# Optimization experiments

Measured on AMD Instinct MI355X. Metric: run time of the kernel, lower is better.

The kernel has to match this reference:

```python
import jax, jax.numpy as jnp
import numpy as np

NUM_HEADS = 8
NUM_Q = 64
RANK = 64
DIM = 768
LN_EPS = 1e-5


def setup_inputs() -> dict:
    key = jax.random.key(0)
    ks = jax.random.split(key, 8)
    b, n = 4, 1024
    x = jax.random.normal(ks[0], (b, NUM_Q, DIM), dtype=jnp.float32)
    context = jax.random.normal(ks[1], (b, n, DIM), dtype=jnp.float32)
    s = 0.02
    Wq = jax.random.normal(ks[2], (DIM, DIM), dtype=jnp.float32) * s
    Wk = jax.random.normal(ks[3], (DIM, DIM), dtype=jnp.float32) * s
    Wv1 = jax.random.normal(ks[4], (DIM, NUM_Q * RANK), dtype=jnp.float32) * s
    ln_g = jnp.ones((NUM_Q * RANK,), dtype=jnp.float32)
    ln_b = jnp.zeros((NUM_Q * RANK,), dtype=jnp.float32)
    Wc = jax.random.normal(ks[5], (NUM_Q, RANK, DIM), dtype=jnp.float32) * s
    Wout = jax.random.normal(ks[6], (DIM, DIM), dtype=jnp.float32) * s
    return {"x": x, "context": context, "Wq": Wq, "Wk": Wk, "Wv1": Wv1,
            "ln_g": ln_g, "ln_b": ln_b, "Wc": Wc, "Wout": Wout}


def reference(x, context, Wq, Wk, Wv1, ln_g, ln_b, Wc, Wout):
    b, nq, d = x.shape
    n = context.shape[1]
    h, dh = NUM_HEADS, d // NUM_HEADS

    q = x @ Wq                      # [b, nq, d]
    k = context @ Wk                # [b, n, d]

    # q-aware V: Linear -> LayerNorm(all_q_mid) -> grouped 1x1 conv (per-query rank->d)
    h1 = context @ Wv1              # [b, n, NUM_Q*RANK]
    mu = jnp.mean(h1, axis=-1, keepdims=True)
    var = jnp.var(h1, axis=-1, keepdims=True)
    h1 = (h1 - mu) * jax.lax.rsqrt(var + LN_EPS) * ln_g + ln_b
    vmid = h1.reshape(b, n, NUM_Q, RANK)
    v = jnp.einsum('bnqr,qrd->bqnd', vmid, Wc)   # [b, NUM_Q, n, d]
    # split heads: 'b q n (h dh) -> b h q n dh'
    v = v.reshape(b, NUM_Q, n, h, dh).transpose(0, 3, 1, 2, 4)

    qh = q.reshape(b, nq, h, dh).transpose(0, 2, 1, 3)   # [b,h,nq,dh]
    kh = k.reshape(b, n, h, dh).transpose(0, 2, 1, 3)    # [b,h,n,dh]
    scale = dh ** (-0.25)
    sim = jnp.einsum('bhid,bhjd->bhij', qh * scale, kh * scale)
    attn = jax.nn.softmax(sim, axis=-1)                  # [b,h,nq,n]
    out = jnp.einsum('bhij,bhijd->bhid', attn, v)        # per-query V
    out = out.transpose(0, 2, 1, 3).reshape(b, nq, d)
    return out @ Wout
```

## Files before the change

### kernel.cpp

```cpp
#include <hip/hip_runtime.h>
#include <math.h>

typedef unsigned short ushort_t;
typedef __bf16 bf16x8 __attribute__((ext_vector_type(8)));
typedef float f32x4 __attribute__((ext_vector_type(4)));

__device__ __forceinline__ ushort_t f2b_rne(float f) {
    union { float f; unsigned int u; } c;
    c.f = f;
    unsigned int u = c.u;
    u += 0x7FFFu + ((u >> 16) & 1u);
    return (ushort_t)(u >> 16);
}
__device__ __forceinline__ float b2f(ushort_t v) {
    union { unsigned int u; float f; } c;
    c.u = ((unsigned int)v) << 16;
    return c.f;
}

__device__ __forceinline__ void gl_lds16(const ushort_t* g, ushort_t* l) {
    __builtin_amdgcn_global_load_lds(
        (const __attribute__((address_space(1))) void*)g,
        (__attribute__((address_space(3))) void*)l, 16, 0, 0);
}

__global__ __launch_bounds__(256) void prep(
    const float* __restrict__ x, const float* __restrict__ context,
    const float* __restrict__ Wq, const float* __restrict__ Wk,
    const float* __restrict__ Wv1, const float* __restrict__ Wout,
    ushort_t* __restrict__ x_b, ushort_t* __restrict__ ctx_b,
    ushort_t* __restrict__ Wq_t, ushort_t* __restrict__ Wk_t,
    ushort_t* __restrict__ Wv1_t, ushort_t* __restrict__ Wout_b,
    float* __restrict__ colzero,
    int b, int n) {
    const int t = threadIdx.x;
    const int bid = blockIdx.x;
    const int nb_x = (b * 64 * 768 / 4) / 256;
    const int nb_c = (b * n * 768 / 4) / 256;

    if (bid < nb_x + nb_c) {
        const float* in = (bid < nb_x) ? x : context;
        ushort_t* outp = (bid < nb_x) ? x_b : ctx_b;
        const int i = ((bid < nb_x) ? bid : (bid - nb_x)) * 256 + t;
        float4 v = ((const float4*)in)[i];
        ushort_t o[4] = {f2b_rne(v.x), f2b_rne(v.y), f2b_rne(v.z), f2b_rne(v.w)};
        *(uint2*)&outp[(size_t)i * 4] = *(uint2*)o;
        return;
    }

    int u = bid - nb_x - nb_c;
    if (u >= 4800) {
        const int idx = (u - 4800) * 256 + t;
        ((float4*)colzero)[idx] = make_float4(0.f, 0.f, 0.f, 0.f);
        return;
    }
    if (u >= 4224) {
        const int i = (u - 4224) * 256 + t;
        float4 v = ((const float4*)Wout)[i];
        ushort_t o[4] = {f2b_rne(v.x), f2b_rne(v.y), f2b_rne(v.z), f2b_rne(v.w)};
        *(uint2*)&Wout_b[(size_t)i * 4] = *(uint2*)o;
        return;
    }

    const float* in;
    ushort_t* outp;
    int R = 768, C = 768;
    if (u < 576)        { in = Wq;  outp = Wq_t; }
    else if (u < 1152)  { u -= 576;  in = Wk;  outp = Wk_t; }
    else                { u -= 1152; in = Wv1; outp = Wv1_t; C = 4096; }
    const int ct = C / 32;
    const int c0 = (u % ct) * 32, r0 = (u / ct) * 32;
    const int tx = t & 31, ty = t >> 5;

    __shared__ float tt[32][33];
#pragma unroll
    for (int i = 0; i < 4; i++)
        tt[ty + 8 * i][tx] = in[(size_t)(r0 + ty + 8 * i) * C + c0 + tx];
    __syncthreads();
#pragma unroll
    for (int i = 0; i < 4; i++)
        outp[(size_t)(c0 + ty + 8 * i) * R + r0 + tx] = f2b_rne(tt[tx][ty + 8 * i]);
}

__global__ __launch_bounds__(256) void gemm3(
    const ushort_t* __restrict__ x_b, const ushort_t* __restrict__ ctx_b,
    const ushort_t* __restrict__ Wq_t, const ushort_t* __restrict__ Wk_t,
    const ushort_t* __restrict__ Wv1_t,
    ushort_t* __restrict__ qb, ushort_t* __restrict__ kb,
    ushort_t* __restrict__ h1t, int b, int n) {
    const int bid = blockIdx.x;
    const int tq = (b * 64 / 128) * 6;
    const int tk = (b * n / 128) * 6;
    const int Mn = b * n;

    const ushort_t *A, *Bt;
    ushort_t* C;
    int N, row0, col0;
    if (bid < tq) {
        A = x_b; Bt = Wq_t; C = qb; N = 768;
        row0 = (bid / 6) * 128; col0 = (bid % 6) * 128;
    } else if (bid < tq + tk) {
        const int u = bid - tq;
        A = ctx_b; Bt = Wk_t; C = kb; N = 768;
        row0 = (u / 6) * 128; col0 = (u % 6) * 128;
    } else {
        const int u = bid - tq - tk;
        A = Wv1_t; Bt = ctx_b; C = h1t; N = Mn;
        row0 = (u % 32) * 128; col0 = (u / 32) * 128;
    }
    const int K = 768;

    __shared__ ushort_t As[2 * 128 * 32];
    __shared__ ushort_t Bs[2 * 128 * 32];

    const int t = threadIdx.x;
    const int lane = t & 63;
    const int wave = t >> 6;
    const int quad = lane >> 4;
    const int l15 = lane & 15;
    const int wm = (wave >> 1) * 64;
    const int wn = (wave & 1) * 64;

    const ushort_t* gA0 = A + (size_t)(row0 + (t >> 2)) * K + (t & 3) * 8;
    const ushort_t* gA1 = gA0 + (size_t)64 * K;
    const ushort_t* gB0 = Bt + (size_t)(col0 + (t >> 2)) * K + (t & 3) * 8;
    const ushort_t* gB1 = gB0 + (size_t)64 * K;

    ushort_t* lA0 = &As[wave * 512];
    ushort_t* lA1 = &As[2048 + wave * 512];
    ushort_t* lA2 = &As[4096 + wave * 512];
    ushort_t* lA3 = &As[6144 + wave * 512];
    ushort_t* lB0 = &Bs[wave * 512];
    ushort_t* lB1 = &Bs[2048 + wave * 512];
    ushort_t* lB2 = &Bs[4096 + wave * 512];
    ushort_t* lB3 = &Bs[6144 + wave * 512];

    f32x4 acc[4][4] = {};

    for (int k0 = 0; k0 < K; k0 += 64) {
        __syncthreads();
        gl_lds16(gA0 + k0, lA0);
        gl_lds16(gA1 + k0, lA1);
        gl_lds16(gA0 + k0 + 32, lA2);
        gl_lds16(gA1 + k0 + 32, lA3);
        gl_lds16(gB0 + k0, lB0);
        gl_lds16(gB1 + k0, lB1);
        gl_lds16(gB0 + k0 + 32, lB2);
        gl_lds16(gB1 + k0 + 32, lB3);
        __syncthreads();

#pragma unroll
        for (int ks = 0; ks < 2; ks++) {
            bf16x8 af[4], bfr[4];
#pragma unroll
            for (int i = 0; i < 4; i++)
                af[i] = *(const bf16x8*)&As[ks * 4096 + (wm + i * 16 + l15) * 32 + quad * 8];
#pragma unroll
            for (int j = 0; j < 4; j++)
                bfr[j] = *(const bf16x8*)&Bs[ks * 4096 + (wn + j * 16 + l15) * 32 + quad * 8];
#pragma unroll
            for (int i = 0; i < 4; i++)
#pragma unroll
                for (int j = 0; j < 4; j++)
                    acc[i][j] = __builtin_amdgcn_mfma_f32_16x16x32_bf16(
                        af[i], bfr[j], acc[i][j], 0, 0, 0);
        }
    }

#pragma unroll
    for (int i = 0; i < 4; i++)
#pragma unroll
        for (int j = 0; j < 4; j++)
#pragma unroll
            for (int r = 0; r < 4; r++) {
                const int row = row0 + wm + i * 16 + quad * 4 + r;
                const int col = col0 + wn + j * 16 + l15;
                C[(size_t)row * N + col] = f2b_rne(acc[i][j][r]);
            }
}

__global__ __launch_bounds__(256) void scores_stats(
    const ushort_t* __restrict__ qb, const ushort_t* __restrict__ kb,
    const ushort_t* __restrict__ h1t, float* __restrict__ S,
    float* __restrict__ colsum, float* __restrict__ colsumsq,
    int b, int n, int Mn) {
    __shared__ ushort_t sb[192 * 104];
    const int t = threadIdx.x;
    const int nsc = b * 8 * (n / 128);

    if (blockIdx.x >= nsc) {
        const int u = blockIdx.x - nsc;
        const int rc = u >> 4;
        const int cc = u & 15;
        const int cg = t & 31;
        const int rg = t >> 5;
        const ushort_t* p =
            h1t + (size_t)(rc * 256 + rg * 32) * Mn + cc * 256 + cg * 8;
        float s[8] = {}, s2[8] = {};
#pragma unroll 4
        for (int r = 0; r < 32; r++) {
            const bf16x8 v = *(const bf16x8*)&p[(size_t)r * Mn];
#pragma unroll
            for (int j = 0; j < 8; j++) {
                const float f = (float)v[j];
                s[j] += f;
                s2[j] += f * f;
            }
        }
        float* red = (float*)sb;
#pragma unroll
        for (int j = 0; j < 8; j++) {
            red[rg * 256 + cg * 8 + j] = s[j];
            red[2048 + rg * 256 + cg * 8 + j] = s2[j];
        }
        __syncthreads();
        float ts = 0.f, ts2 = 0.f;
#pragma unroll
        for (int g = 0; g < 8; g++) {
            ts += red[g * 256 + t];
            ts2 += red[2048 + g * 256 + t];
        }
        atomicAdd(&colsum[cc * 256 + t], ts);
        atomicAdd(&colsumsq[cc * 256 + t], ts2);
        return;
    }

    const int nt = n / 128;
    const int n0 = (blockIdx.x % nt) * 128;
    const int bh = blockIdx.x / nt;
    const int bb = bh >> 3, h = bh & 7;
    const int lane = t & 63, wave = t >> 6;
    const int quad = lane >> 4, l15 = lane & 15;
    const int wm = (wave >> 1) * 32;
    const int wn = (wave & 1) * 64;

    ushort_t* Qs = sb;
    ushort_t* Ks = sb + 64 * 104;

    for (int g = t; g < 768; g += 256) {
        const int r = g / 12, s = g - r * 12;
        *(bf16x8*)&Qs[r * 104 + s * 8] =
            *(const bf16x8*)&qb[(size_t)(bb * 64 + r) * 768 + h * 96 + s * 8];
    }
    for (int g = t; g < 1536; g += 256) {
        const int r = g / 12, s = g - r * 12;
        *(bf16x8*)&Ks[r * 104 + s * 8] =
            *(const bf16x8*)&kb[(size_t)(bb * n + n0 + r) * 768 + h * 96 + s * 8];
    }
    __syncthreads();

    f32x4 acc[2][4] = {};
#pragma unroll
    for (int ks = 0; ks < 3; ks++) {
        bf16x8 af[2], bfr[4];
#pragma unroll
        for (int i = 0; i < 2; i++)
            af[i] = *(const bf16x8*)&Qs[(wm + i * 16 + l15) * 104 + ks * 32 + quad * 8];
#pragma unroll
        for (int j = 0; j < 4; j++)
            bfr[j] = *(const bf16x8*)&Ks[(wn + j * 16 + l15) * 104 + ks * 32 + quad * 8];
#pragma unroll
        for (int i = 0; i < 2; i++)
#pragma unroll
            for (int j = 0; j < 4; j++)
                acc[i][j] = __builtin_amdgcn_mfma_f32_16x16x32_bf16(
                    af[i], bfr[j], acc[i][j], 0, 0, 0);
    }

    const float sc = 0.10206207261596575f;
    float* Sp = S + (size_t)bh * 64 * n;
#pragma unroll
    for (int i = 0; i < 2; i++)
#pragma unroll
        for (int j = 0; j < 4; j++)
#pragma unroll
            for (int r = 0; r < 4; r++) {
                const int row = wm + i * 16 + quad * 4 + r;
                const int col = n0 + wn + j * 16 + l15;
                Sp[(size_t)row * n + col] = acc[i][j][r] * sc;
            }
}

__global__ __launch_bounds__(1024) void attn_fused(
    const float* __restrict__ S, const float* __restrict__ colsum,
    const float* __restrict__ colsumsq, const ushort_t* __restrict__ h1t,
    const float* __restrict__ ln_g, const float* __restrict__ ln_b,
    const float* __restrict__ Wc, const ushort_t* __restrict__ Wout_b,
    float* __restrict__ out, int n, int Mn) {
    const int bq = blockIdx.x;
    const int bb = bq >> 6, qi = bq & 63;
    const int tid = threadIdx.x;
    const int lane = tid & 63, wv = tid >> 6;
    const int quad = lane >> 4, l15 = lane & 15;

    __shared__ ushort_t sW[9 * 1032];
    __shared__ ushort_t sH[64 * 264];
    __shared__ float sl[8], swmu[8];
    __shared__ float pm[16], pl[16], pwm[16];
    __shared__ float sA[512];
    __shared__ float sO[768];

    float* sMu = (float*)sH;
    float* sRs = (float*)sH + 1024;

    for (int i = tid; i < n; i += 1024) {
        const float cs = colsum[bb * n + i];
        const float cq = colsumsq[bb * n + i];
        const float m = cs * (1.0f / 4096.0f);
        sMu[i] = m;
        sRs[i] = rsqrtf(cq * (1.0f / 4096.0f) - m * m + 1e-5f);
    }
    for (int i = tid; i < 1032; i += 1024) sW[8 * 1032 + i] = 0;
    __syncthreads();

    const int h = wv >> 1;
    const int half = wv & 1;
    const int nh = n >> 1;
    const int i0 = half * nh;
    const float* Sp = S + ((size_t)(bb * 8 + h) * 64 + qi) * n;
    {
        float m = -1e30f;
        for (int i = i0 + lane; i < i0 + nh; i += 64) m = fmaxf(m, Sp[i]);
#pragma unroll
        for (int off = 32; off > 0; off >>= 1) m = fmaxf(m, __shfl_down(m, off));
        if (lane == 0) pm[wv] = m;
    }
    __syncthreads();
    const float mh = fmaxf(pm[2 * h], pm[2 * h + 1]);
    {
        float l = 0.f, wm = 0.f;
        for (int i = i0 + lane; i < i0 + nh; i += 64) {
            const float e = expf(Sp[i] - mh);
            const float w = e * sRs[i];
            const ushort_t wb = f2b_rne(w);
            sW[h * 1032 + i] = wb;
            l += e;
            wm += b2f(wb) * sMu[i];
        }
#pragma unroll
        for (int off = 32; off > 0; off >>= 1) {
            l += __shfl_down(l, off);
            wm += __shfl_down(wm, off);
        }
        if (lane == 0) { pl[wv] = l; pwm[wv] = wm; }
    }
    __syncthreads();
    if (tid < 8) {
        sl[tid] = pl[2 * tid] + pl[2 * tid + 1];
        swmu[tid] = pwm[2 * tid] + pwm[2 * tid + 1];
    }

    const int mrow = (l15 < 8 ? l15 : 8) * 1032;
    f32x4 acc = {};
    const int nch = n >> 8;
    for (int ch = 0; ch < nch; ch++) {
        __syncthreads();
        for (int g = tid; g < 2048; g += 1024) {
            const int row = g >> 5, seg = g & 31;
            *(bf16x8*)&sH[row * 264 + seg * 8] =
                *(const bf16x8*)&h1t[(size_t)(qi * 64 + row) * Mn + bb * n +
                                     ch * 256 + seg * 8];
        }
        __syncthreads();
        if (wv < 4) {
#pragma unroll
            for (int ks = 0; ks < 8; ks++) {
                const bf16x8 af = *(const bf16x8*)&sW[mrow + ch * 256 + ks * 32 + quad * 8];
                const bf16x8 bf = *(const bf16x8*)&sH[(wv * 16 + l15) * 264 + ks * 32 + quad * 8];
                acc = __builtin_amdgcn_mfma_f32_16x16x32_bf16(af, bf, acc, 0, 0, 0);
            }
        }
    }
    __syncthreads();

    if (wv < 4) {
#pragma unroll
        for (int r = 0; r < 4; r++) {
            const int hh = quad * 4 + r;
            if (hh < 8) {
                const int rr = wv * 16 + l15;
                const int c = qi * 64 + rr;
                sA[hh * 64 + rr] =
                    ln_g[c] * ((acc[r] - swmu[hh]) / sl[hh]) + ln_b[c];
            }
        }
    }
    __syncthreads();

    for (int d = tid; d < 768; d += 1024) {
        const int hh = d / 96;
        const float* wp = Wc + (size_t)qi * 49152 + d;
        float a = 0.f;
#pragma unroll
        for (int r = 0; r < 64; r++) a += sA[hh * 64 + r] * wp[(size_t)r * 768];
        sO[d] = b2f(f2b_rne(a));
    }
    __syncthreads();

    float* rbuf = (float*)sH;
    if (tid < 768) {
        const int r0 = tid / 96;
        const int c0 = (tid % 96) * 8;
        const ushort_t* wp = Wout_b + (size_t)(r0 * 96) * 768 + c0;
        float acc8[8] = {};
#pragma unroll 4
        for (int s = 0; s < 96; s++) {
            const float sv = sO[r0 * 96 + s];
            const bf16x8 w8 = *(const bf16x8*)&wp[(size_t)s * 768];
#pragma unroll
            for (int j = 0; j < 8; j++) acc8[j] += sv * (float)w8[j];
        }
#pragma unroll
        for (int j = 0; j < 8; j++) rbuf[r0 * 768 + c0 + j] = acc8[j];
    }
    __syncthreads();
    if (tid < 768) {
        float s = 0.f;
#pragma unroll
        for (int g = 0; g < 8; g++) s += rbuf[g * 768 + tid];
        out[(size_t)bq * 768 + tid] = s;
    }
}

extern "C" void kernel_launch(void* const* d_in, const int* in_sizes, int n_in,
                              void* d_out, int out_size, void* d_ws, size_t ws_size,
                              hipStream_t stream) {
    const float* x       = (const float*)d_in[0];
    const float* context = (const float*)d_in[1];
    const float* Wq      = (const float*)d_in[2];
    const float* Wk      = (const float*)d_in[3];
    const float* Wv1     = (const float*)d_in[4];
    const float* ln_g    = (const float*)d_in[5];
    const float* ln_b    = (const float*)d_in[6];
    const float* Wc      = (const float*)d_in[7];
    const float* Wout    = (const float*)d_in[8];
    float* out = (float*)d_out;

    const int b = in_sizes[0] / (64 * 768);
    const int n = in_sizes[1] / (b * 768);
    const int M  = b * 64;
    const int Mn = b * n;

    float* ws = (float*)d_ws;
    size_t off = 0;
    float* S       = ws + off;  off += (size_t)b * 8 * 64 * n;
    float* colsum  = ws + off;  off += (size_t)Mn;
    float* colsumsq= ws + off;  off += (size_t)Mn;

    ushort_t* us = (ushort_t*)(ws + off);
    size_t uo = 0;
    ushort_t* x_b    = us + uo;  uo += (size_t)M * 768;
    ushort_t* ctx_b  = us + uo;  uo += (size_t)Mn * 768;
    ushort_t* qb     = us + uo;  uo += (size_t)M * 768;
    ushort_t* kb     = us + uo;  uo += (size_t)Mn * 768;
    ushort_t* h1t    = us + uo;  uo += (size_t)Mn * 4096;
    ushort_t* Wq_t   = us + uo;  uo += (size_t)768 * 768;
    ushort_t* Wk_t   = us + uo;  uo += (size_t)768 * 768;
    ushort_t* Wv1_t  = us + uo;  uo += (size_t)4096 * 768;
    ushort_t* Wout_b = us + uo;  uo += (size_t)768 * 768;

    const int nb_x = (M * 768 / 4) / 256;
    const int nb_c = (Mn * 768 / 4) / 256;
    prep<<<nb_x + nb_c + 4800 + 8, 256, 0, stream>>>(
        x, context, Wq, Wk, Wv1, Wout, x_b, ctx_b, Wq_t, Wk_t, Wv1_t, Wout_b,
        colsum, b, n);

    const int tq = (M / 128) * 6, tk = (Mn / 128) * 6;
    const int th = (4096 / 128) * (Mn / 128);
    gemm3<<<tq + tk + th, 256, 0, stream>>>(x_b, ctx_b, Wq_t, Wk_t, Wv1_t,
                                            qb, kb, h1t, b, n);

    scores_stats<<<b * 8 * (n / 128) + 256, 256, 0, stream>>>(
        qb, kb, h1t, S, colsum, colsumsq, b, n, Mn);

    attn_fused<<<M, 1024, 0, stream>>>(S, colsum, colsumsq, h1t, ln_g, ln_b,
                                       Wc, Wout_b, out, n, Mn);
}
```

Baseline: 169.7 us.

## Rewrite projection GEMMs with 4-slot LDS ring pipeline and 256x256 tiles

Replaces the double-barrier 128x128 GEMM with a templated tile routine that streams K in 32-wide stages through a four-slot LDS ring, prefetching three stages ahead with explicit vmcnt waits. The big h1 projection uses 256x256 tiles with 512 threads, and the LDS layout is XOR-swizzled to reduce bank conflicts. The aim is to hide global-to-LDS latency and raise MFMA utilisation. In exchange it needs 128KB of dynamic LDS and relies on hand-set wait counts that must match the number of outstanding loads.

```diff
diff --git a/kernel.cpp b/kernel.cpp
--- a/kernel.cpp
+++ b/kernel.cpp
@@ -82,101 +82,141 @@
         outp[(size_t)(c0 + ty + 8 * i) * R + r0 + tx] = f2b_rne(tt[tx][ty + 8 * i]);
 }
 
-__global__ __launch_bounds__(256) void gemm3(
+template <int BM, int BN>
+__device__ __forceinline__ void gemm_tile(
+    const ushort_t* __restrict__ A, const ushort_t* __restrict__ Bt,
+    ushort_t* __restrict__ C, int N, int row0, int col0, ushort_t* lds) {
+    constexpr int K = 768;
+    constexpr int NSTEP = 24;
+    constexpr int SLOT = (BM + BN) * 32;
+    constexpr int AW = BM / 128;
+    constexpr int BW = BN / 128;
+    constexpr int MI = BM / 32;
+    constexpr int NJ = BN / 64;
+
+    const int t = threadIdx.x;
+    const int lane = t & 63, wave = t >> 6;
+    const int quad = lane >> 4, l15 = lane & 15;
+    const int wm = (wave >> 2) * (BM / 2);
+    const int wn = (wave & 3) * (BN / 4);
+
+    const int srow = lane >> 2;
+    const int sslot = (lane & 3) ^ ((lane >> 3) & 3);
+    const ushort_t* gA =
+        A + (size_t)(row0 + wave * (AW * 16) + srow) * K + sslot * 8;
+    const ushort_t* gB =
+        Bt + (size_t)(col0 + wave * (BW * 16) + srow) * K + sslot * 8;
+    const int ldsA = wave * (AW * 512);
+    const int ldsB = BM * 32 + wave * (BW * 512);
+
+    const int rslot = (quad ^ ((l15 >> 1) & 3)) * 8;
+    const int abase = (wm + l15) * 32 + rslot;
+    const int bbase = BM * 32 + (wn + l15) * 32 + rslot;
+
+    f32x4 acc[MI][NJ] = {};
+
+    auto STAGE = [&](int s) {
+        const int rg = (s & 3) * SLOT;
+        const int ko = s * 32;
+        gl_lds16(gA + ko, lds + rg + ldsA);
+        if constexpr (AW == 2) gl_lds16(gA + 16 * K + ko, lds + rg + ldsA + 512);
+        gl_lds16(gB + ko, lds + rg + ldsB);
+        if constexpr (BW == 2) gl_lds16(gB + 16 * K + ko, lds + rg + ldsB + 512);
+    };
+
+    auto COMPUTE = [&](int s) {
+        const int rg = (s & 3) * SLOT;
+        const ushort_t* pA = lds + rg + abase;
+        const ushort_t* pB = lds + rg + bbase;
+        bf16x8 af[MI], bfr[NJ];
+#pragma unroll
+        for (int i = 0; i < MI; ++i) af[i] = *(const bf16x8*)&pA[i * 512];
+#pragma unroll
+        for (int j = 0; j < NJ; ++j) bfr[j] = *(const bf16x8*)&pB[j * 512];
+        __builtin_amdgcn_s_setprio(1);
+#pragma unroll
+        for (int i = 0; i < MI; ++i)
+#pragma unroll
+            for (int j = 0; j < NJ; ++j)
+                acc[i][j] = __builtin_amdgcn_mfma_f32_16x16x32_bf16(
+                    af[i], bfr[j], acc[i][j], 0, 0, 0);
+        __builtin_amdgcn_s_setprio(0);
+    };
+
+    STAGE(0); STAGE(1); STAGE(2);
+
+    for (int s = 0; s < NSTEP - 3; ++s) {
+        __builtin_amdgcn_sched_barrier(0);
+        __builtin_amdgcn_s_barrier();
+        STAGE(s + 3);
+        if constexpr (BM == 256)
+            asm volatile("s_waitcnt vmcnt(12)" ::: "memory");
+        else
+            asm volatile("s_waitcnt vmcnt(6)" ::: "memory");
+        __builtin_amdgcn_s_barrier();
+        __builtin_amdgcn_sched_barrier(0);
+        COMPUTE(s);
+    }
+    __builtin_amdgcn_sched_barrier(0);
+    __builtin_amdgcn_s_barrier();
+    if constexpr (BM == 256) asm volatile("s_waitcnt vmcnt(8)" ::: "memory");
+    else                     asm volatile("s_waitcnt vmcnt(4)" ::: "memory");
+    __builtin_amdgcn_s_barrier();
+    __builtin_amdgcn_sched_barrier(0);
+    COMPUTE(NSTEP - 3);
+
+    __builtin_amdgcn_sched_barrier(0);
+    __builtin_amdgcn_s_barrier();
+    if constexpr (BM == 256) asm volatile("s_waitcnt vmcnt(4)" ::: "memory");
+    else                     asm volatile("s_waitcnt vmcnt(2)" ::: "memory");
+    __builtin_amdgcn_s_barrier();
+    __builtin_amdgcn_sched_barrier(0);
+    COMPUTE(NSTEP - 2);
+
+    __builtin_amdgcn_sched_barrier(0);
+    __builtin_amdgcn_s_barrier();
+    asm volatile("s_waitcnt vmcnt(0)" ::: "memory");
+    __builtin_amdgcn_s_barrier();
+    __builtin_amdgcn_sched_barrier(0);
+    COMPUTE(NSTEP - 1);
+
+#pragma unroll
+    for (int i = 0; i < MI; ++i)
+#pragma unroll
+        for (int j = 0; j < NJ; ++j)
+#pragma unroll
+            for (int r = 0; r < 4; ++r) {
+                const int row = row0 + wm + i * 16 + quad * 4 + r;
+                const int col = col0 + wn + j * 16 + l15;
+                C[(size_t)row * N + col] = f2b_rne(acc[i][j][r]);
+            }
+}
+
+__global__ __launch_bounds__(512, 2) void gemm_ring(
     const ushort_t* __restrict__ x_b, const ushort_t* __restrict__ ctx_b,
     const ushort_t* __restrict__ Wq_t, const ushort_t* __restrict__ Wk_t,
     const ushort_t* __restrict__ Wv1_t,
     ushort_t* __restrict__ qb, ushort_t* __restrict__ kb,
     ushort_t* __restrict__ h1t, int b, int n) {
-    const int bid = blockIdx.x;
-    const int tq = (b * 64 / 128) * 6;
-    const int tk = (b * n / 128) * 6;
+    extern __shared__ ushort_t lds[];
     const int Mn = b * n;
-
-    const ushort_t *A, *Bt;
-    ushort_t* C;
-    int N, row0, col0;
-    if (bid < tq) {
-        A = x_b; Bt = Wq_t; C = qb; N = 768;
-        row0 = (bid / 6) * 128; col0 = (bid % 6) * 128;
-    } else if (bid < tq + tk) {
-        const int u = bid - tq;
-        A = ctx_b; Bt = Wk_t; C = kb; N = 768;
-        row0 = (u / 6) * 128; col0 = (u % 6) * 128;
+    const int M = b * 64;
+    const int nbig = 16 * (Mn / 256);
+    const int nk = (Mn / 128) * 6;
+    int u = blockIdx.x;
+    if (u < nbig) {
+        gemm_tile<256, 256>(Wv1_t, ctx_b, h1t, Mn,
+                            (u & 15) * 256, (u >> 4) * 256, lds);
+    } else if ((u -= nbig) < nk) {
+        const int rt = Mn / 128;
+        gemm_tile<128, 128>(ctx_b, Wk_t, kb, 768,
+                            (u % rt) * 128, (u / rt) * 128, lds);
     } else {
-        const int u = bid - tq - tk;
-        A = Wv1_t; Bt = ctx_b; C = h1t; N = Mn;
-        row0 = (u % 32) * 128; col0 = (u / 32) * 128;
-    }
-    const int K = 768;
-
-    __shared__ ushort_t As[2 * 128 * 32];
-    __shared__ ushort_t Bs[2 * 128 * 32];
-
-    const int t = threadIdx.x;
-    const int lane = t & 63;
-    const int wave = t >> 6;
-    const int quad = lane >> 4;
-    const int l15 = lane & 15;
-    const int wm = (wave >> 1) * 64;
-    const int wn = (wave & 1) * 64;
-
-    const ushort_t* gA0 = A + (size_t)(row0 + (t >> 2)) * K + (t & 3) * 8;
-    const ushort_t* gA1 = gA0 + (size_t)64 * K;
-    const ushort_t* gB0 = Bt + (size_t)(col0 + (t >> 2)) * K + (t & 3) * 8;
-    const ushort_t* gB1 = gB0 + (size_t)64 * K;
-
-    ushort_t* lA0 = &As[wave * 512];
-    ushort_t* lA1 = &As[2048 + wave * 512];
-    ushort_t* lA2 = &As[4096 + wave * 512];
-    ushort_t* lA3 = &As[6144 + wave * 512];
-    ushort_t* lB0 = &Bs[wave * 512];
-    ushort_t* lB1 = &Bs[2048 + wave * 512];
-    ushort_t* lB2 = &Bs[4096 + wave * 512];
-    ushort_t* lB3 = &Bs[6144 + wave * 512];
-
-    f32x4 acc[4][4] = {};
-
-    for (int k0 = 0; k0 < K; k0 += 64) {
-        __syncthreads();
-        gl_lds16(gA0 + k0, lA0);
-        gl_lds16(gA1 + k0, lA1);
-        gl_lds16(gA0 + k0 + 32, lA2);
-        gl_lds16(gA1 + k0 + 32, lA3);
-        gl_lds16(gB0 + k0, lB0);
-        gl_lds16(gB1 + k0, lB1);
-        gl_lds16(gB0 + k0 + 32, lB2);
-        gl_lds16(gB1 + k0 + 32, lB3);
-        __syncthreads();
-
-#pragma unroll
-        for (int ks = 0; ks < 2; ks++) {
-            bf16x8 af[4], bfr[4];
-#pragma unroll
-            for (int i = 0; i < 4; i++)
-                af[i] = *(const bf16x8*)&As[ks * 4096 + (wm + i * 16 + l15) * 32 + quad * 8];
-#pragma unroll
-            for (int j = 0; j < 4; j++)
-                bfr[j] = *(const bf16x8*)&Bs[ks * 4096 + (wn + j * 16 + l15) * 32 + quad * 8];
-#pragma unroll
-            for (int i = 0; i < 4; i++)
-#pragma unroll
-                for (int j = 0; j < 4; j++)
-                    acc[i][j] = __builtin_amdgcn_mfma_f32_16x16x32_bf16(
-                        af[i], bfr[j], acc[i][j], 0, 0, 0);
-        }
-    }
-
-#pragma unroll
-    for (int i = 0; i < 4; i++)
-#pragma unroll
-        for (int j = 0; j < 4; j++)
-#pragma unroll
-            for (int r = 0; r < 4; r++) {
-                const int row = row0 + wm + i * 16 + quad * 4 + r;
-                const int col = col0 + wn + j * 16 + l15;
-                C[(size_t)row * N + col] = f2b_rne(acc[i][j][r]);
-            }
+        u -= nk;
+        const int rt = M / 128;
+        gemm_tile<128, 128>(x_b, Wq_t, qb, 768,
+                            (u % rt) * 128, (u / rt) * 128, lds);
+    }
 }
 
 __global__ __launch_bounds__(256) void scores_stats(
@@ -465,10 +505,18 @@
         x, context, Wq, Wk, Wv1, Wout, x_b, ctx_b, Wq_t, Wk_t, Wv1_t, Wout_b,
         colsum, b, n);
 
-    const int tq = (M / 128) * 6, tk = (Mn / 128) * 6;
-    const int th = (4096 / 128) * (Mn / 128);
-    gemm3<<<tq + tk + th, 256, 0, stream>>>(x_b, ctx_b, Wq_t, Wk_t, Wv1_t,
-                                            qb, kb, h1t, b, n);
+    const int nbig = 16 * (Mn / 256);
+    const int nk = (Mn / 128) * 6;
+    const int nq = (M / 128) * 6;
+    static bool attr_done = false;
+    if (!attr_done) {
+        (void)hipFuncSetAttribute(reinterpret_cast<const void*>(&gemm_ring),
+                                  hipFuncAttributeMaxDynamicSharedMemorySize,
+                                  131072);
+        attr_done = true;
+    }
+    gemm_ring<<<nbig + nk + nq, 512, 131072, stream>>>(
+        x_b, ctx_b, Wq_t, Wk_t, Wv1_t, qb, kb, h1t, b, n);
 
     scores_stats<<<b * 8 * (n / 128) + 256, 256, 0, stream>>>(
         qb, kb, h1t, S, colsum, colsumsq, b, n, Mn);
```

Result: no change. 169.1 us (-0.4%).
